# Performance work log

Hardware: AMD Instinct MI355X
Metric: run time of the kernel (lower is better)

The kernel has to match this reference:

```python
import jax, jax.numpy as jnp
from jax import lax
import numpy as np


def conv4d(x, w, b, pad):
    """4D conv (stride 1) as a sum of 3D convs over the first-spatial-dim kernel taps.
    x: [B, Cin, T, D, H, W]; w: [Cout, Cin, Kt, Kd, Kh, Kw]; same pad on all dims."""
    B, Cin, T, D, H, W = x.shape
    Cout, _, Kt = w.shape[:3]
    xp = jnp.pad(x, ((0, 0), (0, 0), (pad, pad), (0, 0), (0, 0), (0, 0)))
    Tout = T + 2 * pad - Kt + 1
    acc = None
    for k in range(Kt):  # loop over kernel taps (<=3), not data dims
        xs = xp[:, :, k:k + Tout]                      # [B,Cin,Tout,D,H,W]
        xs = xs.transpose(0, 2, 1, 3, 4, 5).reshape(B * Tout, Cin, D, H, W)
        y = lax.conv_general_dilated(
            xs, w[:, :, k], (1, 1, 1), [(pad, pad)] * 3,
            dimension_numbers=('NCDHW', 'OIDHW', 'NCDHW'))
        acc = y if acc is None else acc + y
    Do, Ho, Wo = acc.shape[2:]
    out = acc.reshape(B, Tout, Cout, Do, Ho, Wo).transpose(0, 2, 1, 3, 4, 5)
    return out + b[None, :, None, None, None, None]


def tconv4d_k2s2(x, w, b):
    """4D transposed conv, kernel=2, stride=2, pad=0 (non-overlapping blocks).
    x: [B,Cin,T,D,H,W]; w: [Cin,Cout,2,2,2,2] (PyTorch ConvTranspose layout)."""
    B, Cin, T, D, H, W = x.shape
    Cout = w.shape[1]
    y = jnp.einsum('bcijkl,copqrs->boipjqkrls', x, w)
    y = y.reshape(B, Cout, 2 * T, 2 * D, 2 * H, 2 * W)
    return y + b[None, :, None, None, None, None]


def setup_inputs() -> dict:
    key = jax.random.key(0)
    ks = jax.random.split(key, 10)
    Cin, Cout = 64, 32
    x1 = jax.random.normal(ks[0], (2, Cin, 8, 8, 8, 8), dtype=jnp.float32)
    x2 = jax.random.normal(ks[1], (2, Cin // 2, 16, 16, 16, 16), dtype=jnp.float32)
    def w(k, shape, fan_in):
        return jax.random.normal(k, shape, dtype=jnp.float32) / np.float32(np.sqrt(fan_in))
    up_w = w(ks[2], (Cin, Cin // 2, 2, 2, 2, 2), Cin * 16)
    up_b = w(ks[3], (Cin // 2,), Cin * 16)
    w1 = w(ks[4], (Cout, Cin, 3, 3, 3, 3), Cin * 81)
    b1 = w(ks[5], (Cout,), Cin * 81)
    w2 = w(ks[6], (Cout, Cout, 3, 3, 3, 3), Cout * 81)
    b2 = w(ks[7], (Cout,), Cout * 81)
    w3 = w(ks[8], (Cout, Cin, 1, 1, 1, 1), Cin)
    b3 = w(ks[9], (Cout,), Cin)
    return {'x1': x1, 'x2': x2, 'up_w': up_w, 'up_b': up_b,
            'w1': w1, 'b1': b1, 'w2': w2, 'b2': b2, 'w3': w3, 'b3': b3}


def reference(x1, x2, up_w, up_b, w1, b1, w2, b2, w3, b3):
    x1u = tconv4d_k2s2(x1, up_w, up_b)              # [B, Cin//2, 16,16,16,16]
    xc = jnp.concatenate([x2, x1u], axis=1)          # [B, Cin, 16,16,16,16]
    Y = jax.nn.relu(conv4d(xc, w1, b1, 1))
    Y = conv4d(Y, w2, b2, 1)
    sc = conv4d(xc, w3, b3, 0)                       # 1x1 residual projection
    return jax.nn.relu(Y + sc)
```

## Files before the change

kernel.cpp:

```cpp
#include <hip/hip_runtime.h>

typedef unsigned short u16;
typedef __attribute__((ext_vector_type(8))) short short8;
typedef __attribute__((ext_vector_type(4))) float f32x4;

#define XCB_OFF  0
#define Y1B_OFF  8388608
#define W1P_OFF  12582912
#define W2P_OFF  12748800
#define W3P_OFF  12831744
#define UPWP_OFF 12833792
#define ZPAD_OFF 12866560

__device__ __forceinline__ u16 f2bf(float v) {
    unsigned u = __builtin_bit_cast(unsigned, v);
    u += 0x7FFFu + ((u >> 16) & 1u);
    return (u16)(u >> 16);
}

__device__ __forceinline__ f32x4 MFMA(short8 a, short8 b, f32x4 c) {
    return __builtin_amdgcn_mfma_f32_16x16x32_bf16(a, b, c, 0, 0, 0);
}

typedef const __attribute__((address_space(1))) u16 gas_u16;
typedef __attribute__((address_space(3))) u16 las_u16;
__device__ __forceinline__ void gload16(const u16* g, u16* l) {
    __builtin_amdgcn_global_load_lds((gas_u16*)g, (las_u16*)l, 16, 0, 0);
}

__global__ __launch_bounds__(256) void setup(const float* __restrict__ w1,
                                             const float* __restrict__ w2,
                                             const float* __restrict__ w3,
                                             const float* __restrict__ upw,
                                             const float* __restrict__ x2,
                                             u16* __restrict__ ws) {
    __shared__ u16 lds[256 * 40];
    int bid = blockIdx.x;
    int tid = threadIdx.x;
    if (bid == 0 && tid < 64) ws[ZPAD_OFF + tid] = 0;
    if (bid < 512) {
        int b = bid >> 8;
        int pos_base = (bid & 255) * 256;
        u16* xcb = ws + XCB_OFF;
        #pragma unroll
        for (int c = 0; c < 32; ++c) {
            lds[tid * 40 + c] = f2bf(x2[((b * 32 + c) << 16) + pos_base + tid]);
        }
        __syncthreads();
        #pragma unroll
        for (int k = 0; k < 4; ++k) {
            int f = k * 256 + tid;
            int u = f & 3, pos = f >> 2;
            uint4 v = *(const uint4*)(lds + pos * 40 + u * 8);
            *(uint4*)(xcb + (size_t)((b << 16) + pos_base + pos) * 64 + u * 8) = v;
        }
    } else {
        int idx = (bid - 512) * 256 + tid;
        if (idx < 165888) {
            int j = idx & 7, lane = (idx >> 3) & 63, rest = idx >> 9;
            int half = rest & 1, chunk = (rest >> 1) & 1, tap = rest >> 2;
            int co = half * 16 + (lane & 15), ci = chunk * 32 + (lane >> 4) * 8 + j;
            ws[W1P_OFF + idx] = f2bf(w1[(co * 64 + ci) * 81 + tap]);
        } else if (idx < 165888 + 82944) {
            int i2 = idx - 165888;
            int j = i2 & 7, lane = (i2 >> 3) & 63, rest = i2 >> 9;
            int half = rest & 1, tap = rest >> 1;
            int co = half * 16 + (lane & 15), ci = (lane >> 4) * 8 + j;
            ws[W2P_OFF + i2] = f2bf(w2[(co * 32 + ci) * 81 + tap]);
        } else if (idx < 165888 + 82944 + 2048) {
            int i3 = idx - (165888 + 82944);
            int j = i3 & 7, lane = (i3 >> 3) & 63, rest = i3 >> 9;
            int half = rest & 1, chunk = rest >> 1;
            int co = half * 16 + (lane & 15), ci = chunk * 32 + (lane >> 4) * 8 + j;
            ws[W3P_OFF + i3] = f2bf(w3[co * 64 + ci]);
        } else if (idx < 250880 + 32768) {
            int i4 = idx - 250880;
            int j = i4 & 7, lane = (i4 >> 3) & 63, rest = i4 >> 9;
            int half = rest & 1, chunk = (rest >> 1) & 1, tap = rest >> 2;
            int co = half * 16 + (lane & 15), ci = chunk * 32 + (lane >> 4) * 8 + j;
            ws[UPWP_OFF + i4] = f2bf(upw[(ci * 32 + co) * 16 + tap]);
        }
    }
}

__global__ __launch_bounds__(256) void xc_up_mfma(const float* __restrict__ x1,
                                                  const u16* __restrict__ upwp,
                                                  const float* __restrict__ up_b,
                                                  u16* __restrict__ xcb) {
    __shared__ u16 lds[64 * 72];
    int tid = threadIdx.x;
    int wv = tid >> 6, lane = tid & 63;
    int q = lane >> 4, m = lane & 15;
    int bid = blockIdx.x;
    int tp = bid & 1, j = (bid >> 1) & 63, b = bid >> 7;
    int pos_base = j * 64;

    #pragma unroll
    for (int g = 0; g < 16; ++g) {
        int c = g * 4 + wv;
        lds[lane * 72 + c] = f2bf(x1[((b * 64 + c) << 12) + pos_base + lane]);
    }
    __syncthreads();

    const short8* wv8 = (const short8*)upwp;
    float4 bi0 = ((const float4*)up_b)[q];
    float4 bi1 = ((const float4*)up_b)[4 + q];
    int it = j >> 3, id = j & 7;

    for (int tt = 0; tt < 2; ++tt) {
        int tap = tp * 8 + wv * 2 + tt;
        f32x4 acc[4][2];
        #pragma unroll
        for (int g = 0; g < 4; ++g) {
            acc[g][0] = (f32x4){bi0.x, bi0.y, bi0.z, bi0.w};
            acc[g][1] = (f32x4){bi1.x, bi1.y, bi1.z, bi1.w};
        }
        #pragma unroll
        for (int chunk = 0; chunk < 2; ++chunk) {
            short8 a0 = wv8[((tap * 2 + chunk) * 2 + 0) * 64 + lane];
            short8 a1 = wv8[((tap * 2 + chunk) * 2 + 1) * 64 + lane];
            #pragma unroll
            for (int g = 0; g < 4; ++g) {
                short8 bf = *(const short8*)(lds + (g * 16 + m) * 72 + chunk * 32 + q * 8);
                acc[g][0] = MFMA(a0, bf, acc[g][0]);
                acc[g][1] = MFMA(a1, bf, acc[g][1]);
            }
        }
        int pt = tap >> 3, pd = (tap >> 2) & 1, ph = (tap >> 1) & 1, pw = tap & 1;
        int oT = 2 * it + pt, oD = 2 * id + pd, oW = 2 * (m & 7) + pw;
        #pragma unroll
        for (int g = 0; g < 4; ++g) {
            int ih = g * 2 + (m >> 3);
            int opos = oT * 4096 + oD * 256 + (2 * ih + ph) * 16 + oW;
            u16* op = xcb + (size_t)((b << 16) + opos) * 64 + 32 + q * 4;
            #pragma unroll
            for (int half = 0; half < 2; ++half) {
                f32x4 v = acc[g][half];
                uint2 o;
                o.x = (unsigned)f2bf(v.x) | ((unsigned)f2bf(v.y) << 16);
                o.y = (unsigned)f2bf(v.z) | ((unsigned)f2bf(v.w) << 16);
                *(uint2*)(op + half * 16) = o;
            }
        }
    }
}

__global__ __launch_bounds__(256, 2) void conv1_mfma(const u16* __restrict__ xcb,
                                                     const u16* __restrict__ w1p,
                                                     const float* __restrict__ b1,
                                                     const u16* __restrict__ zpad,
                                                     u16* __restrict__ y1b) {
    __shared__ __attribute__((aligned(16))) u16 lds[27648];
    int tid = threadIdx.x;
    int lane = tid & 63, wv = tid >> 6;
    int q = lane >> 4, m = lane & 15;
    int c = wv & 1, hf = wv >> 1;
    int bid = blockIdx.x;
    int xcd = bid & 7;
    int b = xcd >> 2, tq = xcd & 3;
    int loc = bid >> 3;
    int hB = loc & 1;
    int d = (loc >> 1) & 15;
    int tl = (loc >> 5) & 3;
    int t = tq * 4 + tl;
    int h0 = hB * 8;
    int rot = (bid * 5) % 9;

    int gofs[6], lofs[6];
    bool st[6], inr[6];
    #pragma unroll
    for (int k = 0; k < 6; ++k) {
        int ui = tid + k * 256;
        int hh = ui / 144, rem = ui - hh * 144;
        int p = rem >> 3, w = rem & 7;
        int u_src = w ^ (p & 7);
        int gh = h0 - 1 + hh, gw = p - 1;
        st[k] = ui < 1440;
        inr[k] = st[k] && ((unsigned)gh < 16u) && ((unsigned)gw < 16u);
        gofs[k] = (gh * 16 + gw) * 64 + u_src * 8;
        lofs[k] = ui * 8;
    }

    f32x4 acc[8];
    if (c == 0) {
        float4 bi = ((const float4*)b1)[hf * 4 + q];
        #pragma unroll
        for (int i = 0; i < 8; ++i)
            acc[i] = (f32x4){bi.x, bi.y, bi.z, bi.w};
    } else {
        #pragma unroll
        for (int i = 0; i < 8; ++i)
            acc[i] = (f32x4){0.f, 0.f, 0.f, 0.f};
    }
    const short8* w1v = (const short8*)w1p;

    auto issue_plane = [&](int ktd, int bb) {
        int kt = ktd / 3, kd = ktd - kt * 3;
        int tt = t + kt - 1, dd = d + kd - 1;
        bool pv = ((unsigned)tt < 16u) && ((unsigned)dd < 16u);
        const u16* src = xcb + (size_t)(((b * 16 + tt) * 16 + dd)) * 16384;
        #pragma unroll
        for (int k = 0; k < 6; ++k) {
            if (st[k]) {
                const u16* g = (pv && inr[k]) ? (src + gofs[k]) : zpad;
                gload16(g, lds + bb * 13824 + lofs[k]);
            }
        }
    };

    issue_plane(rot, 0);
    for (int s = 0; s < 9; ++s) {
        int ktd = rot + s; if (ktd >= 9) ktd -= 9;
        int kt = ktd / 3, kd = ktd - kt * 3;
        __syncthreads();
        short8 W[3][3];
        #pragma unroll
        for (int kw = 0; kw < 3; ++kw)
            #pragma unroll
            for (int kh = 0; kh < 3; ++kh) {
                int tap = ((kt * 3 + kd) * 3 + kh) * 3 + kw;
                W[kw][kh] = w1v[((tap * 2 + c) * 2 + hf) * 64 + lane];
            }
        __builtin_amdgcn_sched_barrier(0);
        if (s < 8) {
            int nk = ktd + 1; if (nk >= 9) nk -= 9;
            issue_plane(nk, (s + 1) & 1);
        }
        __builtin_amdgcn_sched_barrier(0);
        const u16* L = lds + (s & 1) * 13824;
        __builtin_amdgcn_s_setprio(1);
        #pragma unroll
        for (int kw = 0; kw < 3; ++kw) {
            int p = kw + m, pm = p & 7;
            int bo = p * 64 + ((((c << 2) | q) ^ pm) << 3);
            short8 R[10];
            #pragma unroll
            for (int r = 0; r < 10; ++r)
                R[r] = *(const short8*)(L + r * 1152 + bo);
            #pragma unroll
            for (int kh = 0; kh < 3; ++kh) {
                #pragma unroll
                for (int i = 0; i < 8; ++i)
                    acc[i] = MFMA(W[kw][kh], R[i + kh], acc[i]);
            }
        }
        __builtin_amdgcn_s_setprio(0);
    }

    __syncthreads();
    f32x4* buf = (f32x4*)lds;
    if (c == 1) {
        #pragma unroll
        for (int i = 0; i < 8; ++i)
            buf[(hf * 8 + i) * 64 + lane] = acc[i];
    }
    __syncthreads();
    if (c == 0) {
        int obase = ((b * 16 + t) * 16 + d) * 256 + h0 * 16 + m;
        #pragma unroll
        for (int i = 0; i < 8; ++i) {
            int pos = obase + i * 16;
            f32x4 v = acc[i];
            f32x4 w = buf[(hf * 8 + i) * 64 + lane];
            v.x += w.x; v.y += w.y; v.z += w.z; v.w += w.w;
            unsigned r0 = f2bf(fmaxf(v.x, 0.f)), r1 = f2bf(fmaxf(v.y, 0.f));
            unsigned r2 = f2bf(fmaxf(v.z, 0.f)), r3 = f2bf(fmaxf(v.w, 0.f));
            uint2 o;
            o.x = r0 | (r1 << 16);
            o.y = r2 | (r3 << 16);
            *(uint2*)(y1b + (size_t)pos * 32 + hf * 16 + q * 4) = o;
        }
    }
}

__global__ __launch_bounds__(256, 2) void conv2_mfma(const u16* __restrict__ y1b,
                                                     const u16* __restrict__ xcb,
                                                     const u16* __restrict__ w2p,
                                                     const u16* __restrict__ w3p,
                                                     const float* __restrict__ b2,
                                                     const float* __restrict__ b3,
                                                     const u16* __restrict__ zpad,
                                                     float* __restrict__ out) {
    __shared__ __attribute__((aligned(16))) u16 lds[20736];
    int tid = threadIdx.x;
    int lane = tid & 63, wv = tid >> 6;
    int q = lane >> 4, m = lane & 15;
    int hf = wv & 1, rh = wv >> 1;
    int bid = blockIdx.x;
    int xcd = bid & 7;
    int b = xcd >> 2, tq = xcd & 3;
    int loc = bid >> 3;
    int d = loc & 15;
    int tl = (loc >> 4) & 3;
    int t = tq * 4 + tl;
    int rot = (bid * 5) % 9;

    int gofs[6], lofs[6];
    bool st[6], inr[6];
    #pragma unroll
    for (int k = 0; k < 6; ++k) {
        int ui = tid + k * 256;
        int hh = ui / 72, rem = ui - hh * 72;
        int p = rem >> 2, w = rem & 3;
        int u_src = w ^ (p & 3);
        int gh = hh - 1, gw = p - 1;
        st[k] = ui < 1296;
        inr[k] = st[k] && ((unsigned)gh < 16u) && ((unsigned)gw < 16u);
        gofs[k] = (gh * 16 + gw) * 32 + u_src * 8;
        lofs[k] = ui * 8;
    }

    f32x4 acc[8];
    {
        float4 p0 = ((const float4*)b2)[hf * 4 + q];
        float4 s0 = ((const float4*)b3)[hf * 4 + q];
        #pragma unroll
        for (int i = 0; i < 8; ++i)
            acc[i] = (f32x4){p0.x + s0.x, p0.y + s0.y, p0.z + s0.z, p0.w + s0.w};
    }
    const short8* w2v = (const short8*)w2p;

    auto issue_plane = [&](int ktd, int bb) {
        int kt = ktd / 3, kd = ktd - kt * 3;
        int tt = t + kt - 1, dd = d + kd - 1;
        bool pv = ((unsigned)tt < 16u) && ((unsigned)dd < 16u);
        const u16* src = y1b + (size_t)(((b * 16 + tt) * 16 + dd)) * 8192;
        #pragma unroll
        for (int k = 0; k < 6; ++k) {
            if (st[k]) {
                const u16* g = (pv && inr[k]) ? (src + gofs[k]) : zpad;
                gload16(g, lds + bb * 10368 + lofs[k]);
            }
        }
    };

    issue_plane(rot, 0);
    for (int s = 0; s < 9; ++s) {
        int ktd = rot + s; if (ktd >= 9) ktd -= 9;
        __syncthreads();
        short8 W[3][3];
        #pragma unroll
        for (int kw = 0; kw < 3; ++kw)
            #pragma unroll
            for (int kh = 0; kh < 3; ++kh) {
                int tap = (ktd * 3 + kh) * 3 + kw;
                W[kw][kh] = w2v[(tap * 2 + hf) * 64 + lane];
            }
        __builtin_amdgcn_sched_barrier(0);
        if (s < 8) {
            int nk = ktd + 1; if (nk >= 9) nk -= 9;
            issue_plane(nk, (s + 1) & 1);
        }
        __builtin_amdgcn_sched_barrier(0);
        const u16* L = lds + (s & 1) * 10368;
        __builtin_amdgcn_s_setprio(1);
        #pragma unroll
        for (int kw = 0; kw < 3; ++kw) {
            int p = kw + m, pm = p & 3;
            int bo = p * 32 + ((q ^ pm) << 3);
            short8 R[10];
            #pragma unroll
            for (int r = 0; r < 10; ++r)
                R[r] = *(const short8*)(L + (rh * 8 + r) * 576 + bo);
            #pragma unroll
            for (int kh = 0; kh < 3; ++kh) {
                #pragma unroll
                for (int i = 0; i < 8; ++i)
                    acc[i] = MFMA(W[kw][kh], R[i + kh], acc[i]);
            }
        }
        __builtin_amdgcn_s_setprio(0);
    }

    const short8* w3v = (const short8*)w3p;
    int lpos0 = (t * 16 + d) * 256 + (rh * 8) * 16 + m;
    int gpos0 = (b << 16) + lpos0;
    #pragma unroll
    for (int chunk = 0; chunk < 2; ++chunk) {
        short8 a = w3v[(chunk * 2 + hf) * 64 + lane];
        #pragma unroll
        for (int i = 0; i < 8; ++i) {
            short8 bf = *(const short8*)(xcb + (size_t)(gpos0 + i * 16) * 64 + ((chunk << 2) | q) * 8);
            acc[i] = MFMA(a, bf, acc[i]);
        }
    }

    #pragma unroll
    for (int i = 0; i < 8; ++i) {
        int lpos = lpos0 + i * 16;
        f32x4 v = acc[i];
        int co = hf * 16 + q * 4;
        float* op = out + (((size_t)(b * 32 + co)) << 16) + lpos;
        op[0ull << 16] = fmaxf(v.x, 0.f);
        op[1ull << 16] = fmaxf(v.y, 0.f);
        op[2ull << 16] = fmaxf(v.z, 0.f);
        op[3ull << 16] = fmaxf(v.w, 0.f);
    }
}

extern "C" void kernel_launch(void* const* d_in, const int* in_sizes, int n_in,
                              void* d_out, int out_size, void* d_ws, size_t ws_size,
                              hipStream_t stream) {
    const float* x1   = (const float*)d_in[0];
    const float* x2   = (const float*)d_in[1];
    const float* up_w = (const float*)d_in[2];
    const float* up_b = (const float*)d_in[3];
    const float* w1   = (const float*)d_in[4];
    const float* b1   = (const float*)d_in[5];
    const float* w2   = (const float*)d_in[6];
    const float* b2   = (const float*)d_in[7];
    const float* w3   = (const float*)d_in[8];
    const float* b3   = (const float*)d_in[9];
    u16* ws  = (u16*)d_ws;
    float* out = (float*)d_out;

    setup<<<1620, 256, 0, stream>>>(w1, w2, w3, up_w, x2, ws);
    xc_up_mfma<<<256, 256, 0, stream>>>(x1, ws + UPWP_OFF, up_b, ws + XCB_OFF);
    conv1_mfma<<<1024, 256, 0, stream>>>(ws + XCB_OFF, ws + W1P_OFF, b1,
                                         ws + ZPAD_OFF, ws + Y1B_OFF);
    conv2_mfma<<<512, 256, 0, stream>>>(ws + Y1B_OFF, ws + XCB_OFF, ws + W2P_OFF,
                                        ws + W3P_OFF, b2, b3, ws + ZPAD_OFF, out);
}
```

Baseline: 155.3 us.

## Triple-buffer conv1 LDS planes and prefetch weights one stage ahead

Conv1's input-plane staging goes from double to triple buffering, so two planes are in flight at once. Explicit vmcnt waits replace the full __syncthreads, and the next tap's weights are prefetched into registers during the current stage's MFMAs. The ui<1440 store guard is dropped, so every slot now issues a load, with out-of-range slots reading zpad, which keeps the vmcnt counts uniform. This adds LDS use (36864 u16) and registers for the second weight set, which may lower occupancy under launch_bounds(256,2). The hand-counted vmcnt values are fragile.

```diff
diff --git a/kernel.cpp b/kernel.cpp
--- a/kernel.cpp
+++ b/kernel.cpp
@@ -150,7 +150,7 @@
                                                      const float* __restrict__ b1,
                                                      const u16* __restrict__ zpad,
                                                      u16* __restrict__ y1b) {
-    __shared__ __attribute__((aligned(16))) u16 lds[27648];
+    __shared__ __attribute__((aligned(16))) u16 lds[36864];
     int tid = threadIdx.x;
     int lane = tid & 63, wv = tid >> 6;
     int q = lane >> 4, m = lane & 15;
@@ -167,7 +167,7 @@
     int rot = (bid * 5) % 9;
 
     int gofs[6], lofs[6];
-    bool st[6], inr[6];
+    bool inr[6];
     #pragma unroll
     for (int k = 0; k < 6; ++k) {
         int ui = tid + k * 256;
@@ -175,8 +175,7 @@
         int p = rem >> 3, w = rem & 7;
         int u_src = w ^ (p & 7);
         int gh = h0 - 1 + hh, gw = p - 1;
-        st[k] = ui < 1440;
-        inr[k] = st[k] && ((unsigned)gh < 16u) && ((unsigned)gw < 16u);
+        inr[k] = (ui < 1440) && ((unsigned)gh < 16u) && ((unsigned)gw < 16u);
         gofs[k] = (gh * 16 + gw) * 64 + u_src * 8;
         lofs[k] = ui * 8;
     }
@@ -201,33 +200,53 @@
         const u16* src = xcb + (size_t)(((b * 16 + tt) * 16 + dd)) * 16384;
         #pragma unroll
         for (int k = 0; k < 6; ++k) {
-            if (st[k]) {
-                const u16* g = (pv && inr[k]) ? (src + gofs[k]) : zpad;
-                gload16(g, lds + bb * 13824 + lofs[k]);
-            }
+            const u16* g = (pv && inr[k]) ? (src + gofs[k]) : zpad;
+            gload16(g, lds + bb * 12288 + lofs[k]);
         }
     };
 
+    short8 Wc[3][3], Wn[3][3];
     issue_plane(rot, 0);
+    __builtin_amdgcn_sched_barrier(0);
+    {
+        int kt = rot / 3, kd = rot - kt * 3;
+        #pragma unroll
+        for (int kw = 0; kw < 3; ++kw)
+            #pragma unroll
+            for (int kh = 0; kh < 3; ++kh) {
+                int tap = ((kt * 3 + kd) * 3 + kh) * 3 + kw;
+                Wc[kw][kh] = w1v[((tap * 2 + c) * 2 + hf) * 64 + lane];
+            }
+    }
+    __builtin_amdgcn_sched_barrier(0);
+    { int nk = rot + 1; if (nk >= 9) nk -= 9; issue_plane(nk, 1); }
+    __builtin_amdgcn_sched_barrier(0);
+
     for (int s = 0; s < 9; ++s) {
         int ktd = rot + s; if (ktd >= 9) ktd -= 9;
-        int kt = ktd / 3, kd = ktd - kt * 3;
-        __syncthreads();
-        short8 W[3][3];
-        #pragma unroll
-        for (int kw = 0; kw < 3; ++kw)
-            #pragma unroll
-            for (int kh = 0; kh < 3; ++kh) {
-                int tap = ((kt * 3 + kd) * 3 + kh) * 3 + kw;
-                W[kw][kh] = w1v[((tap * 2 + c) * 2 + hf) * 64 + lane];
-            }
+        if (s == 8) { asm volatile("s_waitcnt vmcnt(9)" ::: "memory"); }
+        else        { asm volatile("s_waitcnt vmcnt(15)" ::: "memory"); }
+        __builtin_amdgcn_sched_barrier(0);
+        __builtin_amdgcn_s_barrier();
         __builtin_amdgcn_sched_barrier(0);
         if (s < 8) {
             int nk = ktd + 1; if (nk >= 9) nk -= 9;
-            issue_plane(nk, (s + 1) & 1);
-        }
-        __builtin_amdgcn_sched_barrier(0);
-        const u16* L = lds + (s & 1) * 13824;
+            int kt = nk / 3, kd = nk - kt * 3;
+            #pragma unroll
+            for (int kw = 0; kw < 3; ++kw)
+                #pragma unroll
+                for (int kh = 0; kh < 3; ++kh) {
+                    int tap = ((kt * 3 + kd) * 3 + kh) * 3 + kw;
+                    Wn[kw][kh] = w1v[((tap * 2 + c) * 2 + hf) * 64 + lane];
+                }
+        }
+        __builtin_amdgcn_sched_barrier(0);
+        if (s < 7) {
+            int nk2 = ktd + 2; if (nk2 >= 9) nk2 -= 9;
+            issue_plane(nk2, (s + 2) % 3);
+        }
+        __builtin_amdgcn_sched_barrier(0);
+        const u16* L = lds + (s % 3) * 12288;
         __builtin_amdgcn_s_setprio(1);
         #pragma unroll
         for (int kw = 0; kw < 3; ++kw) {
@@ -241,10 +260,17 @@
             for (int kh = 0; kh < 3; ++kh) {
                 #pragma unroll
                 for (int i = 0; i < 8; ++i)
-                    acc[i] = MFMA(W[kw][kh], R[i + kh], acc[i]);
+                    acc[i] = MFMA(Wc[kw][kh], R[i + kh], acc[i]);
             }
         }
         __builtin_amdgcn_s_setprio(0);
+        if (s < 8) {
+            #pragma unroll
+            for (int kw = 0; kw < 3; ++kw)
+                #pragma unroll
+                for (int kh = 0; kh < 3; ++kh)
+                    Wc[kw][kh] = Wn[kw][kh];
+        }
     }
 
     __syncthreads();
```

After: 155.7 us. About the same (+0.3%).
